# Kernel tuning notes

Measured on AMD Instinct MI355X. Metric: run time of the kernel, lower is better.

Reference implementation:

```python
import jax, jax.numpy as jnp
import numpy as np

B, S, H, NH = 8, 1024, 768, 12
DK = H // NH  # 64


def setup_inputs() -> dict:
    key = jax.random.key(0)
    ks = jax.random.split(key, 7)
    sc = 0.02
    return {
        "Q": jax.random.normal(ks[0], (B, S, H), jnp.float32),
        "K": jax.random.normal(ks[1], (B, S, H), jnp.float32),
        "V": jax.random.normal(ks[2], (B, S, H), jnp.float32),
        "Wq": jax.random.normal(ks[3], (H, H), jnp.float32) * sc,
        "Wk": jax.random.normal(ks[4], (H, H), jnp.float32) * sc,
        "Wv": jax.random.normal(ks[5], (H, H), jnp.float32) * sc,
        "Wo": jax.random.normal(ks[6], (H, H), jnp.float32) * sc,
    }


def reference(Q, K, V, Wq, Wk, Wv, Wo):
    # torch Linear(bias=False): y = x @ W.T, weight shape [out, in]
    q = jnp.einsum('bsh,oh->bso', Q, Wq).reshape(B, S, NH, DK)
    k = jnp.einsum('bsh,oh->bso', K, Wk).reshape(B, S, NH, DK)
    v = jnp.einsum('bsh,oh->bso', V, Wv).reshape(B, S, NH, DK)
    # naive SDPA per head: full [B,NH,S,S] score matrix, scale by sqrt(dk)
    scores = jnp.einsum('bqnd,bknd->bnqk', q, k) / jnp.sqrt(jnp.float32(DK))
    w = jax.nn.softmax(scores, axis=-1)
    c = jnp.einsum('bnqk,bknd->bqnd', w, v).reshape(B, S, H)
    return jnp.einsum('bsh,oh->bso', c, Wo)
```

## Files before the change

### kernel.cpp

```cpp
#include <hip/hip_runtime.h>
#include <hip/hip_bf16.h>

#define B_   8
#define S_   1024
#define H_   768
#define NH_  12
#define DK_  64
#define M_   (B_ * S_)

typedef __attribute__((ext_vector_type(8))) short          short8;
typedef __attribute__((ext_vector_type(8))) unsigned short ushort8;
typedef __attribute__((ext_vector_type(4))) unsigned short ushort4v;
typedef __attribute__((ext_vector_type(4))) float          f32x4;

__device__ __forceinline__ unsigned short f2bf(float x) {
    union { __hip_bfloat16 h; unsigned short u; } r;
    r.h = __float2bfloat16(x);
    return r.u;
}

__device__ __forceinline__ unsigned cvtpk_bf16(float lo, float hi) {
    unsigned r;
    asm("v_cvt_pk_bf16_f32 %0, %1, %2" : "=v"(r) : "v"(lo), "v"(hi));
    return r;
}

__device__ __forceinline__ void glds16(const unsigned short* g, unsigned short* l) {
    __builtin_amdgcn_global_load_lds(
        (const __attribute__((address_space(1))) unsigned int*)g,
        (__attribute__((address_space(3))) unsigned int*)l, 16, 0, 0);
}

__global__ __launch_bounds__(256)
void cvt_w(const float* __restrict__ w0, const float* __restrict__ w1,
           const float* __restrict__ w2, const float* __restrict__ w3,
           unsigned short* __restrict__ o0, unsigned short* __restrict__ o1,
           unsigned short* __restrict__ o2, unsigned short* __restrict__ o3)
{
    const int wsel = blockIdx.y;
    const float* src = (wsel == 0) ? w0 : (wsel == 1) ? w1 : (wsel == 2) ? w2 : w3;
    unsigned short* dst = (wsel == 0) ? o0 : (wsel == 1) ? o1 : (wsel == 2) ? o2 : o3;
    const float s = (wsel == 0) ? 0.125f * 1.44269504089f : 1.0f;
    const int i = blockIdx.x * 256 + threadIdx.x;
    const float4 x = ((const float4*)src)[i];
    ushort4v o;
    o[0] = f2bf(x.x * s); o[1] = f2bf(x.y * s);
    o[2] = f2bf(x.z * s); o[3] = f2bf(x.w * s);
    ((ushort4v*)dst)[i] = o;
}

#define GEMM_ISSUE(AsX, BsX, k0)                                              \
  {                                                                           \
    glds16(gB + (k0), (BsX) + w * 512);                                       \
    glds16(gB + (size_t)64 * H_ + (k0), (BsX) + 2048 + w * 512);              \
    if (A_BF16) {                                                             \
      glds16(gAh + (k0), (AsX) + w * 512);                                    \
      glds16(gAh + (size_t)64 * H_ + (k0), (AsX) + 2048 + w * 512);           \
    } else {                                                                  \
      _Pragma("unroll")                                                       \
      for (int i = 0; i < 2; i++) {                                           \
        araw[2 * i]     = *(const float4*)(gAf + (size_t)i * 64 * H_ + (k0)); \
        araw[2 * i + 1] = *(const float4*)(gAf + (size_t)i * 64 * H_ + (k0) + 4);\
      }                                                                       \
    }                                                                         \
  }

#define GEMM_WRITE_A(AsX)                                                     \
  if (!A_BF16) {                                                              \
    _Pragma("unroll")                                                         \
    for (int i = 0; i < 2; i++) {                                             \
      ushort8 o8;                                                             \
      o8[0] = f2bf(araw[2 * i].x);     o8[1] = f2bf(araw[2 * i].y);           \
      o8[2] = f2bf(araw[2 * i].z);     o8[3] = f2bf(araw[2 * i].w);           \
      o8[4] = f2bf(araw[2 * i + 1].x); o8[5] = f2bf(araw[2 * i + 1].y);       \
      o8[6] = f2bf(araw[2 * i + 1].z); o8[7] = f2bf(araw[2 * i + 1].w);       \
      *(ushort8*)&(AsX)[(i * 64 + srow) * 32 + sc8] = o8;                     \
    }                                                                         \
  }

#define GEMM_COMPUTE(AsX, BsX)                                                \
  {                                                                           \
    short8 af[4], bfr[4];                                                     \
    _Pragma("unroll")                                                         \
    for (int mi = 0; mi < 4; mi++)                                            \
      af[mi] = *(const short8*)&(AsX)[(wm + mi * 16 + lc) * 32 + lg * 8];     \
    _Pragma("unroll")                                                         \
    for (int ni = 0; ni < 4; ni++)                                            \
      bfr[ni] = *(const short8*)&(BsX)[(wn + ni * 16 + lc) * 32 + lg * 8];    \
    __builtin_amdgcn_s_setprio(1);                                            \
    _Pragma("unroll")                                                         \
    for (int mi = 0; mi < 4; mi++)                                            \
      _Pragma("unroll")                                                       \
      for (int ni = 0; ni < 4; ni++)                                          \
        acc[mi][ni] = __builtin_amdgcn_mfma_f32_16x16x32_bf16(                \
            af[mi], bfr[ni], acc[mi][ni], 0, 0, 0);                           \
    __builtin_amdgcn_s_setprio(0);                                            \
  }

template<bool A_BF16, bool OUT_BF16>
__global__ __launch_bounds__(256)
void gemm_bt(const void* __restrict__ A0, const void* __restrict__ A1,
             const void* __restrict__ A2,
             const unsigned short* __restrict__ W0,
             const unsigned short* __restrict__ W1,
             const unsigned short* __restrict__ W2,
             void* __restrict__ C0, void* __restrict__ C1, void* __restrict__ C2)
{
    __shared__ unsigned short As0[128 * 32];
    __shared__ unsigned short Bs0[128 * 32];
    __shared__ unsigned short As1[128 * 32];
    __shared__ unsigned short Bs1[128 * 32];

    const int tid  = threadIdx.x;
    const int bid  = blockIdx.x;
    const int x    = bid & 7, j = bid >> 3;
    const int z    = j / 48;
    const int r48  = j % 48;
    const int bm   = x * 8 + r48 / 6;
    const int bn   = r48 % 6;

    const int w    = tid >> 6, lane = tid & 63;
    const int lg   = lane >> 4, lc = lane & 15;
    const int wm   = (w >> 1) * 64, wn = (w & 1) * 64;

    const void* Av = (z == 0) ? A0 : (z == 1) ? A1 : A2;
    const unsigned short* Bw = (z == 0) ? W0 : (z == 1) ? W1 : W2;
    void* Cv = (z == 0) ? C0 : (z == 1) ? C1 : C2;

    const float*          Af = (const float*)Av;
    const unsigned short* Ah = (const unsigned short*)Av;

    const int srow = tid >> 2;
    const int sc8  = (tid & 3) * 8;

    const unsigned short* gB  = &Bw[(size_t)(bn * 128 + srow) * H_ + sc8];
    const unsigned short* gAh = A_BF16 ? &Ah[(size_t)(bm * 128 + srow) * H_ + sc8] : nullptr;
    const float*          gAf = A_BF16 ? nullptr : &Af[(size_t)(bm * 128 + srow) * H_ + sc8];

    f32x4 acc[4][4] = {};
    float4 araw[4];

    GEMM_ISSUE(As0, Bs0, 0);
    GEMM_WRITE_A(As0);
    __syncthreads();

#pragma unroll 1
    for (int t = 0; t < 22; t += 2) {
        GEMM_ISSUE(As1, Bs1, (t + 1) * 32);
        GEMM_COMPUTE(As0, Bs0);
        GEMM_WRITE_A(As1);
        __syncthreads();

        GEMM_ISSUE(As0, Bs0, (t + 2) * 32);
        GEMM_COMPUTE(As1, Bs1);
        GEMM_WRITE_A(As0);
        __syncthreads();
    }

    GEMM_ISSUE(As1, Bs1, 23 * 32);
    GEMM_COMPUTE(As0, Bs0);
    GEMM_WRITE_A(As1);
    __syncthreads();
    GEMM_COMPUTE(As1, Bs1);

#pragma unroll
    for (int mi = 0; mi < 4; mi++)
#pragma unroll
        for (int ni = 0; ni < 4; ni++)
#pragma unroll
            for (int reg = 0; reg < 4; reg++) {
                const int row = bm * 128 + wm + mi * 16 + lg * 4 + reg;
                const int col = bn * 128 + wn + ni * 16 + lc;
                if (OUT_BF16)
                    ((unsigned short*)Cv)[(size_t)row * H_ + col] = f2bf(acc[mi][ni][reg]);
                else
                    ((float*)Cv)[(size_t)row * H_ + col] = acc[mi][ni][reg];
            }
}

__global__ __launch_bounds__(256)
void transpose_v(const unsigned short* __restrict__ v,
                 unsigned short* __restrict__ vt)
{
    __shared__ unsigned short T[64][72];
    const int tid = threadIdx.x;
    const int st0 = blockIdx.x, h = blockIdx.y, b = blockIdx.z;
    const int r = tid >> 2, d0 = (tid & 3) * 16, g = tid & 3;

    const unsigned short* src = &v[(size_t)(b * S_ + st0 * 64 + r) * H_ + h * DK_ + d0];
    const ushort8 v0 = *(const ushort8*)src;
    const ushort8 v1 = *(const ushort8*)(src + 8);
    const int colv = r ^ (g << 4);
#pragma unroll
    for (int jj = 0; jj < 8; jj++) T[d0 + jj][colv]     = v0[jj];
#pragma unroll
    for (int jj = 0; jj < 8; jj++) T[d0 + 8 + jj][colv] = v1[jj];
    __syncthreads();

    const size_t ob = ((size_t)(b * NH_ + h) * DK_) * S_ + st0 * 64;
#pragma unroll
    for (int half = 0; half < 2; half++) {
        const int ci = half * 256 + tid;
        const int d = ci >> 3, kc = ci & 7;
        const int sw = ((d >> 4) & 3) << 4;
        const ushort8 val = *(const ushort8*)&T[d][(kc * 8) ^ sw];
        *(ushort8*)&vt[ob + (size_t)d * S_ + kc * 8] = val;
    }
}

__global__ __launch_bounds__(256)
void attn(const unsigned short* __restrict__ q,
          const unsigned short* __restrict__ k,
          const unsigned short* __restrict__ vt,
          unsigned short* __restrict__ c)
{
    __shared__ unsigned short Ks[64][72];
    __shared__ unsigned short Vs[64][72];

    const int tid  = threadIdx.x;
    const int qt   = blockIdx.x, h = blockIdx.y, b = blockIdx.z;
    const int wid  = tid >> 6;
    const int lane = tid & 63;
    const int lg   = lane >> 4, lc = lane & 15;
    const int r    = tid >> 2;
    const int g    = tid & 3;
    const int d0   = g * 16;
    const size_t base = (size_t)b * S_ * H_ + (size_t)h * DK_;
    const size_t vtb  = (size_t)(b * NH_ + h) * DK_ * S_;

    short8 aq[2][2];
#pragma unroll
    for (int m = 0; m < 2; m++)
#pragma unroll
        for (int ks = 0; ks < 2; ks++)
            aq[m][ks] = *(const short8*)
                &q[base + (size_t)(qt * 128 + wid * 32 + m * 16 + lc) * H_ + ks * 32 + lg * 8];

    f32x4 o[2][4] = {};
    float lsum[2] = {0.f, 0.f};

    for (int kt = 0; kt < S_ / 64; kt++) {
        {
            const unsigned short* ksrc = &k[base + (size_t)(kt * 64 + r) * H_ + d0];
            *(ushort8*)&Ks[r][d0]     = *(const ushort8*)ksrc;
            *(ushort8*)&Ks[r][d0 + 8] = *(const ushort8*)(ksrc + 8);
            const unsigned short* vsrc = &vt[vtb + (size_t)r * S_ + kt * 64 + d0];
            *(ushort8*)&Vs[r][d0]     = *(const ushort8*)vsrc;
            *(ushort8*)&Vs[r][d0 + 8] = *(const ushort8*)(vsrc + 8);
        }
        __syncthreads();

        f32x4 st[2][4] = {};
        __builtin_amdgcn_s_setprio(1);
#pragma unroll
        for (int ni = 0; ni < 4; ni++)
#pragma unroll
            for (int ks = 0; ks < 2; ks++) {
                const short8 bk = *(const short8*)&Ks[ni * 16 + lc][ks * 32 + lg * 8];
                st[0][ni] = __builtin_amdgcn_mfma_f32_16x16x32_bf16(bk, aq[0][ks], st[0][ni], 0, 0, 0);
                st[1][ni] = __builtin_amdgcn_mfma_f32_16x16x32_bf16(bk, aq[1][ks], st[1][ni], 0, 0, 0);
            }
        __builtin_amdgcn_s_setprio(0);

        unsigned pw[2][4][2];
#pragma unroll
        for (int m = 0; m < 2; m++) {
#pragma unroll
            for (int ni = 0; ni < 4; ni++) {
#pragma unroll
                for (int reg = 0; reg < 4; reg++) {
                    const float pp = exp2f(st[m][ni][reg]);
                    st[m][ni][reg] = pp;
                    lsum[m] += pp;
                }
                pw[m][ni][0] = cvtpk_bf16(st[m][ni][0], st[m][ni][1]);
                pw[m][ni][1] = cvtpk_bf16(st[m][ni][2], st[m][ni][3]);
            }
        }

        const int sl0 = lc + ((lg & 1) << 5);
        const int sl1 = sl0 + 16;
        const bool hi = (lg >> 1) != 0;
        short8 pa[2][2];
#pragma unroll
        for (int m = 0; m < 2; m++)
#pragma unroll
            for (int ks = 0; ks < 2; ks++) {
                const unsigned lo0 = pw[m][2 * ks][0],     lo1 = pw[m][2 * ks][1];
                const unsigned hi0 = pw[m][2 * ks + 1][0], hi1 = pw[m][2 * ks + 1][1];
                union { unsigned u[4]; short8 s8; } pk;
                const unsigned a0l = __shfl(lo0, sl0, 64), a0h = __shfl(hi0, sl0, 64);
                const unsigned a1l = __shfl(lo1, sl0, 64), a1h = __shfl(hi1, sl0, 64);
                const unsigned a2l = __shfl(lo0, sl1, 64), a2h = __shfl(hi0, sl1, 64);
                const unsigned a3l = __shfl(lo1, sl1, 64), a3h = __shfl(hi1, sl1, 64);
                pk.u[0] = hi ? a0h : a0l;
                pk.u[1] = hi ? a1h : a1l;
                pk.u[2] = hi ? a2h : a2l;
                pk.u[3] = hi ? a3h : a3l;
                pa[m][ks] = pk.s8;
            }

        __builtin_amdgcn_s_setprio(1);
#pragma unroll
        for (int ni = 0; ni < 4; ni++)
#pragma unroll
            for (int ks = 0; ks < 2; ks++) {
                const short8 bv = *(const short8*)&Vs[ni * 16 + lc][ks * 32 + lg * 8];
                o[0][ni] = __builtin_amdgcn_mfma_f32_16x16x32_bf16(pa[0][ks], bv, o[0][ni], 0, 0, 0);
                o[1][ni] = __builtin_amdgcn_mfma_f32_16x16x32_bf16(pa[1][ks], bv, o[1][ni], 0, 0, 0);
            }
        __builtin_amdgcn_s_setprio(0);
        __syncthreads();
    }

#pragma unroll
    for (int m = 0; m < 2; m++) {
        float l = lsum[m];
        l += __shfl_xor(l, 16, 64);
        l += __shfl_xor(l, 32, 64);
        const float iv = 1.0f / l;
#pragma unroll
        for (int reg = 0; reg < 4; reg++) {
            const float ivr = __shfl(iv, lg * 4 + reg, 64);
            const int row = qt * 128 + wid * 32 + m * 16 + lg * 4 + reg;
#pragma unroll
            for (int ni = 0; ni < 4; ni++)
                c[base + (size_t)row * H_ + ni * 16 + lc] = f2bf(o[m][ni][reg] * ivr);
        }
    }
}

extern "C" void kernel_launch(void* const* d_in, const int* in_sizes, int n_in,
                              void* d_out, int out_size, void* d_ws, size_t ws_size,
                              hipStream_t stream)
{
    const float* Q  = (const float*)d_in[0];
    const float* K  = (const float*)d_in[1];
    const float* V  = (const float*)d_in[2];
    const float* Wq = (const float*)d_in[3];
    const float* Wk = (const float*)d_in[4];
    const float* Wv = (const float*)d_in[5];
    const float* Wo = (const float*)d_in[6];

    unsigned short* qb = (unsigned short*)d_ws;
    unsigned short* kb = qb + (size_t)M_ * H_;
    unsigned short* vb = kb + (size_t)M_ * H_;
    unsigned short* vtb = vb + (size_t)M_ * H_;
    unsigned short* cb  = vb;
    unsigned short* wq = vtb + (size_t)M_ * H_;
    unsigned short* wk = wq + (size_t)H_ * H_;
    unsigned short* wv = wk + (size_t)H_ * H_;
    unsigned short* wo = wv + (size_t)H_ * H_;

    cvt_w<<<dim3(H_ * H_ / 4 / 256, 4), 256, 0, stream>>>(
        Wq, Wk, Wv, Wo, wq, wk, wv, wo);

    gemm_bt<false, true><<<dim3(64 * 6 * 3), 256, 0, stream>>>(
        Q, K, V, wq, wk, wv, qb, kb, vb);

    transpose_v<<<dim3(S_ / 64, NH_, B_), 256, 0, stream>>>(vb, vtb);

    attn<<<dim3(S_ / 128, NH_, B_), 256, 0, stream>>>(qb, kb, vtb, cb);

    gemm_bt<true, false><<<dim3(64 * 6), 256, 0, stream>>>(
        cb, cb, cb, wo, wo, wo, d_out, d_out, d_out);
}
```

Before: 151.6 us.

## Pre-convert activations to bf16 and split QKV projection into separate GEMMs

Adds a standalone fp32-to-bf16 conversion kernel for Q, K and V inputs, so the projection GEMM can always load A tiles asynchronously into LDS instead of loading fp32 into registers and converting inline. The fused three-way QKV GEMM launch becomes three sequential convert+GEMM pairs that reuse one scratch buffer. This trades extra global traffic (writing and re-reading bf16 activations) and more launches with smaller grids for a simpler, fully async GEMM main loop.

```diff
diff --git a/kernel.cpp b/kernel.cpp
--- a/kernel.cpp
+++ b/kernel.cpp
@@ -49,33 +49,23 @@
     ((ushort4v*)dst)[i] = o;
 }
 
+__global__ __launch_bounds__(256)
+void cvt_x(const float* __restrict__ in, unsigned short* __restrict__ out)
+{
+    const int i = blockIdx.x * 256 + threadIdx.x;
+    const float4 x = ((const float4*)in)[i];
+    ushort4v o;
+    o[0] = f2bf(x.x); o[1] = f2bf(x.y);
+    o[2] = f2bf(x.z); o[3] = f2bf(x.w);
+    ((ushort4v*)out)[i] = o;
+}
+
 #define GEMM_ISSUE(AsX, BsX, k0)                                              \
   {                                                                           \
     glds16(gB + (k0), (BsX) + w * 512);                                       \
     glds16(gB + (size_t)64 * H_ + (k0), (BsX) + 2048 + w * 512);              \
-    if (A_BF16) {                                                             \
-      glds16(gAh + (k0), (AsX) + w * 512);                                    \
-      glds16(gAh + (size_t)64 * H_ + (k0), (AsX) + 2048 + w * 512);           \
-    } else {                                                                  \
-      _Pragma("unroll")                                                       \
-      for (int i = 0; i < 2; i++) {                                           \
-        araw[2 * i]     = *(const float4*)(gAf + (size_t)i * 64 * H_ + (k0)); \
-        araw[2 * i + 1] = *(const float4*)(gAf + (size_t)i * 64 * H_ + (k0) + 4);\
-      }                                                                       \
-    }                                                                         \
-  }
-
-#define GEMM_WRITE_A(AsX)                                                     \
-  if (!A_BF16) {                                                              \
-    _Pragma("unroll")                                                         \
-    for (int i = 0; i < 2; i++) {                                             \
-      ushort8 o8;                                                             \
-      o8[0] = f2bf(araw[2 * i].x);     o8[1] = f2bf(araw[2 * i].y);           \
-      o8[2] = f2bf(araw[2 * i].z);     o8[3] = f2bf(araw[2 * i].w);           \
-      o8[4] = f2bf(araw[2 * i + 1].x); o8[5] = f2bf(araw[2 * i + 1].y);       \
-      o8[6] = f2bf(araw[2 * i + 1].z); o8[7] = f2bf(araw[2 * i + 1].w);       \
-      *(ushort8*)&(AsX)[(i * 64 + srow) * 32 + sc8] = o8;                     \
-    }                                                                         \
+    glds16(gAh + (k0), (AsX) + w * 512);                                      \
+    glds16(gAh + (size_t)64 * H_ + (k0), (AsX) + 2048 + w * 512);             \
   }
 
 #define GEMM_COMPUTE(AsX, BsX)                                                \
@@ -97,14 +87,11 @@
     __builtin_amdgcn_s_setprio(0);                                            \
   }
 
-template<bool A_BF16, bool OUT_BF16>
-__global__ __launch_bounds__(256)
-void gemm_bt(const void* __restrict__ A0, const void* __restrict__ A1,
-             const void* __restrict__ A2,
-             const unsigned short* __restrict__ W0,
-             const unsigned short* __restrict__ W1,
-             const unsigned short* __restrict__ W2,
-             void* __restrict__ C0, void* __restrict__ C1, void* __restrict__ C2)
+template<bool OUT_BF16>
+__global__ __launch_bounds__(256)
+void gemm_bt(const unsigned short* __restrict__ Ah,
+             const unsigned short* __restrict__ Bw,
+             void* __restrict__ Cv)
 {
     __shared__ unsigned short As0[128 * 32];
     __shared__ unsigned short Bs0[128 * 32];
@@ -114,7 +101,6 @@
     const int tid  = threadIdx.x;
     const int bid  = blockIdx.x;
     const int x    = bid & 7, j = bid >> 3;
-    const int z    = j / 48;
     const int r48  = j % 48;
     const int bm   = x * 8 + r48 / 6;
     const int bn   = r48 % 6;
@@ -123,43 +109,30 @@
     const int lg   = lane >> 4, lc = lane & 15;
     const int wm   = (w >> 1) * 64, wn = (w & 1) * 64;
 
-    const void* Av = (z == 0) ? A0 : (z == 1) ? A1 : A2;
-    const unsigned short* Bw = (z == 0) ? W0 : (z == 1) ? W1 : W2;
-    void* Cv = (z == 0) ? C0 : (z == 1) ? C1 : C2;
-
-    const float*          Af = (const float*)Av;
-    const unsigned short* Ah = (const unsigned short*)Av;
-
     const int srow = tid >> 2;
     const int sc8  = (tid & 3) * 8;
 
     const unsigned short* gB  = &Bw[(size_t)(bn * 128 + srow) * H_ + sc8];
-    const unsigned short* gAh = A_BF16 ? &Ah[(size_t)(bm * 128 + srow) * H_ + sc8] : nullptr;
-    const float*          gAf = A_BF16 ? nullptr : &Af[(size_t)(bm * 128 + srow) * H_ + sc8];
+    const unsigned short* gAh = &Ah[(size_t)(bm * 128 + srow) * H_ + sc8];
 
     f32x4 acc[4][4] = {};
-    float4 araw[4];
 
     GEMM_ISSUE(As0, Bs0, 0);
-    GEMM_WRITE_A(As0);
     __syncthreads();
 
 #pragma unroll 1
     for (int t = 0; t < 22; t += 2) {
         GEMM_ISSUE(As1, Bs1, (t + 1) * 32);
         GEMM_COMPUTE(As0, Bs0);
-        GEMM_WRITE_A(As1);
         __syncthreads();
 
         GEMM_ISSUE(As0, Bs0, (t + 2) * 32);
         GEMM_COMPUTE(As1, Bs1);
-        GEMM_WRITE_A(As0);
         __syncthreads();
     }
 
     GEMM_ISSUE(As1, Bs1, 23 * 32);
     GEMM_COMPUTE(As0, Bs0);
-    GEMM_WRITE_A(As1);
     __syncthreads();
     GEMM_COMPUTE(As1, Bs1);
 
@@ -342,26 +315,32 @@
     const float* Wv = (const float*)d_in[5];
     const float* Wo = (const float*)d_in[6];
 
-    unsigned short* qb = (unsigned short*)d_ws;
-    unsigned short* kb = qb + (size_t)M_ * H_;
-    unsigned short* vb = kb + (size_t)M_ * H_;
+    unsigned short* qb  = (unsigned short*)d_ws;
+    unsigned short* kb  = qb + (size_t)M_ * H_;
+    unsigned short* vb  = kb + (size_t)M_ * H_;
     unsigned short* vtb = vb + (size_t)M_ * H_;
+    unsigned short* xs  = vtb;
     unsigned short* cb  = vb;
-    unsigned short* wq = vtb + (size_t)M_ * H_;
-    unsigned short* wk = wq + (size_t)H_ * H_;
-    unsigned short* wv = wk + (size_t)H_ * H_;
-    unsigned short* wo = wv + (size_t)H_ * H_;
+    unsigned short* wq  = vtb + (size_t)M_ * H_;
+    unsigned short* wk  = wq + (size_t)H_ * H_;
+    unsigned short* wv  = wk + (size_t)H_ * H_;
+    unsigned short* wo  = wv + (size_t)H_ * H_;
+
+    const int nx = M_ * H_ / 4 / 256;
 
     cvt_w<<<dim3(H_ * H_ / 4 / 256, 4), 256, 0, stream>>>(
         Wq, Wk, Wv, Wo, wq, wk, wv, wo);
 
-    gemm_bt<false, true><<<dim3(64 * 6 * 3), 256, 0, stream>>>(
-        Q, K, V, wq, wk, wv, qb, kb, vb);
+    cvt_x<<<nx, 256, 0, stream>>>(Q, xs);
+    gemm_bt<true ><<<dim3(64 * 6), 256, 0, stream>>>(xs, wq, qb);
+    cvt_x<<<nx, 256, 0, stream>>>(K, xs);
+    gemm_bt<true ><<<dim3(64 * 6), 256, 0, stream>>>(xs, wk, kb);
+    cvt_x<<<nx, 256, 0, stream>>>(V, xs);
+    gemm_bt<true ><<<dim3(64 * 6), 256, 0, stream>>>(xs, wv, vb);
 
     transpose_v<<<dim3(S_ / 64, NH_, B_), 256, 0, stream>>>(vb, vtb);
 
     attn<<<dim3(S_ / 128, NH_, B_), 256, 0, stream>>>(qb, kb, vtb, cb);
 
-    gemm_bt<true, false><<<dim3(64 * 6), 256, 0, stream>>>(
-        cb, cb, cb, wo, wo, wo, d_out, d_out, d_out);
-}
+    gemm_bt<false><<<dim3(64 * 6), 256, 0, stream>>>(cb, wo, (float*)d_out);
+}
```

Result: slower. 177.6 us (+17.2%).
